# Optimization experiments

Hardware: AMD Instinct MI355X
Metric: run time of the kernel (lower is better)

The kernel has to match this reference:

```python
import jax, jax.numpy as jnp
import numpy as np

B, L, E = 2, 2048, 2048
H, KVH, HD = 16, 4, 128          # n_heads, n_kv_heads, head_dim = E // H
WIN = 512                        # window_size
SCALE = 1.0 / (HD ** 0.5)
NEG = -1e30


def setup_inputs() -> dict:
    key = jax.random.key(0)
    ks = jax.random.split(key, 5)
    s = 0.02
    return {
        "x":  jax.random.normal(ks[0], (B, L, E), dtype=jnp.float32),
        "Wq": jax.random.normal(ks[1], (E, H * HD), dtype=jnp.float32) * s,
        "Wk": jax.random.normal(ks[2], (E, KVH * HD), dtype=jnp.float32) * s,
        "Wv": jax.random.normal(ks[3], (E, KVH * HD), dtype=jnp.float32) * s,
        "Wo": jax.random.normal(ks[4], (H * HD, E), dtype=jnp.float32) * s,
    }


def reference(x, Wq, Wk, Wv, Wo):
    # projections
    q = (x @ Wq).reshape(B, L, H, HD)      # [B, L, H, HD]
    k = (x @ Wk).reshape(B, L, KVH, HD)    # [B, L, KVH, HD]
    v = (x @ Wv).reshape(B, L, KVH, HD)
    # GQA: expand kv heads (repeat_interleave over head dim)
    rep = H // KVH
    k = jnp.repeat(k, rep, axis=2)         # [B, L, H, HD]
    v = jnp.repeat(v, rep, axis=2)
    # scores [B, H, L, L]
    scores = jnp.einsum("bqhd,bkhd->bhqk", q, k) * SCALE
    i = jnp.arange(L)[:, None]
    j = jnp.arange(L)[None, :]
    mask = (j > i) | (j < i - WIN)         # True = masked
    scores = jnp.where(mask[None, None], NEG, scores)
    attn = jax.nn.softmax(scores, axis=-1)
    out = jnp.einsum("bhqk,bkhd->bqhd", attn, v).reshape(B, L, H * HD)
    return out @ Wo                        # [B, L, E]
```

## Files before the change

kernel.cpp:

```cpp
#include <hip/hip_runtime.h>
#include <hip/hip_bf16.h>
#include <type_traits>

#define B_ 2
#define L_ 2048
#define E_ 2048
#define H_ 16
#define KVH_ 4
#define HD_ 128
#define WIN_ 512
#define REP_ (H_ / KVH_)
#define SCALE_ 0.08838834764831843f

typedef __bf16 bf16x8 __attribute__((ext_vector_type(8)));
typedef float f32x4 __attribute__((ext_vector_type(4)));
typedef unsigned short u16x8 __attribute__((ext_vector_type(8)));

__device__ __forceinline__ unsigned short f2bf(float x) {
    __hip_bfloat16 h = __float2bfloat16(x);
    return *reinterpret_cast<unsigned short*>(&h);
}

__device__ __forceinline__ void gload_lds16(const unsigned short* g, unsigned short* l) {
    __builtin_amdgcn_global_load_lds(
        (const __attribute__((address_space(1))) void*)g,
        (__attribute__((address_space(3))) void*)l,
        16, 0, 0);
}

__global__ __launch_bounds__(256) void conv_f32_bf16(
        const float* __restrict__ in, unsigned short* __restrict__ out, int n4) {
    int i = blockIdx.x * 256 + threadIdx.x;
    if (i >= n4) return;
    float4 v = reinterpret_cast<const float4*>(in)[i];
    ushort4 o;
    o.x = f2bf(v.x); o.y = f2bf(v.y); o.z = f2bf(v.z); o.w = f2bf(v.w);
    reinterpret_cast<ushort4*>(out)[i] = o;
}

__global__ __launch_bounds__(256) void transpose_f32_bf16(
        const float* __restrict__ W, unsigned short* __restrict__ WT,
        int K, int N, int wts) {
    __shared__ unsigned short tile[32][33];
    const int t = threadIdx.x;
    const int r = t >> 5, c = t & 31;
    const int k0 = blockIdx.y * 32, n0 = blockIdx.x * 32;
    #pragma unroll
    for (int i = 0; i < 4; ++i)
        tile[r + i * 8][c] = f2bf(W[(size_t)(k0 + r + i * 8) * N + n0 + c]);
    __syncthreads();
    #pragma unroll
    for (int i = 0; i < 4; ++i)
        WT[(size_t)(n0 + r + i * 8) * wts + k0 + c] = tile[c][r + i * 8];
}

__global__ __launch_bounds__(256) void transpose_v_bf16(
        const unsigned short* __restrict__ kv, unsigned short* __restrict__ vT) {
    __shared__ unsigned short tile[32][33];
    const int t = threadIdx.x;
    const int r = t >> 5, c = t & 31;
    const int l0 = blockIdx.y * 32;
    const int n0 = blockIdx.x * 32;
    #pragma unroll
    for (int i = 0; i < 4; ++i)
        tile[r + i * 8][c] = kv[(size_t)(l0 + r + i * 8) * 1024 + 512 + n0 + c];
    __syncthreads();
    const int bq = l0 >> 11, lqv = l0 & 2047;
    #pragma unroll
    for (int i = 0; i < 4; ++i)
        vT[(size_t)(bq * 512 + n0 + r + i * 8) * (size_t)L_ + lqv + c] = tile[c][r + i * 8];
}

template<typename OT>
__global__ __launch_bounds__(256) void gemm_bt(
        const unsigned short* __restrict__ A, const unsigned short* __restrict__ BT,
        OT* __restrict__ C, int M, int N, int K) {
    __shared__ __attribute__((aligned(16))) unsigned short As[128 * 32];
    __shared__ __attribute__((aligned(16))) unsigned short Bs[128 * 32];
    const int t  = threadIdx.x;
    const int wv = t >> 6, ln = t & 63;
    const int wr = wv >> 1, wc = wv & 1;
    const int nwg = gridDim.x * gridDim.y;
    int lin = blockIdx.y * gridDim.x + blockIdx.x;
    if ((nwg & 7) == 0) lin = (lin & 7) * (nwg >> 3) + (lin >> 3);
    const int bm = (lin / gridDim.x) * 128, bn = (lin % gridDim.x) * 128;
    const int lrow = ln & 15;
    const int lk8  = (ln >> 4) * 8;

    f32x4 acc[4][4];
    const f32x4 z = {0.f, 0.f, 0.f, 0.f};
    #pragma unroll
    for (int m = 0; m < 4; ++m)
        #pragma unroll
        for (int n = 0; n < 4; ++n) acc[m][n] = z;

    for (int k0 = 0; k0 < K; k0 += 32) {
        #pragma unroll
        for (int seg = 0; seg < 2; ++seg) {
            const int chunk = seg * 256 + t;
            const int row = chunk >> 2, c8 = (chunk & 3) * 8;
            const int lbase = (seg * 256 + wv * 64) * 8;
            gload_lds16(A  + (size_t)(bm + row) * K + k0 + c8, &As[lbase]);
            gload_lds16(BT + (size_t)(bn + row) * K + k0 + c8, &Bs[lbase]);
        }
        __syncthreads();
        bf16x8 af[4], bfr[4];
        #pragma unroll
        for (int m = 0; m < 4; ++m)
            af[m] = *reinterpret_cast<const bf16x8*>(
                &As[(wr * 64 + m * 16 + lrow) * 32 + lk8]);
        #pragma unroll
        for (int n = 0; n < 4; ++n)
            bfr[n] = *reinterpret_cast<const bf16x8*>(
                &Bs[(wc * 64 + n * 16 + lrow) * 32 + lk8]);
        __builtin_amdgcn_s_setprio(1);
        #pragma unroll
        for (int m = 0; m < 4; ++m)
            #pragma unroll
            for (int n = 0; n < 4; ++n)
                acc[m][n] = __builtin_amdgcn_mfma_f32_16x16x32_bf16(
                    af[m], bfr[n], acc[m][n], 0, 0, 0);
        __builtin_amdgcn_s_setprio(0);
        __syncthreads();
    }
    const int crq = (ln >> 4) * 4;
    #pragma unroll
    for (int m = 0; m < 4; ++m)
        #pragma unroll
        for (int n = 0; n < 4; ++n)
            #pragma unroll
            for (int r = 0; r < 4; ++r) {
                size_t idx = (size_t)(bm + wr * 64 + m * 16 + crq + r) * N
                             + bn + wc * 64 + n * 16 + lrow;
                if constexpr (std::is_same_v<OT, float>) C[idx] = acc[m][n][r];
                else C[idx] = f2bf(acc[m][n][r]);
            }
}

__global__ __launch_bounds__(256) void attn_mfma(
        const unsigned short* __restrict__ qb,
        const unsigned short* __restrict__ kvb,
        const unsigned short* __restrict__ vT,
        unsigned short* __restrict__ ob) {
    __shared__ __attribute__((aligned(16))) unsigned short Ks[32 * 128];
    __shared__ __attribute__((aligned(16))) unsigned short VsT[128 * 40];

    const int t  = threadIdx.x;
    const int w  = t >> 6, l = t & 63;
    const int lin = blockIdx.y * gridDim.x + blockIdx.x;
    const int wid = (lin & 7) * 128 + (lin >> 3);
    const int bh  = wid >> 5;
    const int qt  = 31 - (wid & 31);
    const int b  = bh >> 4, h = bh & 15;
    const int kh = h >> 2;
    const int i0 = qt * 64;
    const int iw = i0 + w * 16;
    const int lq = l & 15;
    const int g  = l >> 4;
    const int g8 = g * 8;
    const int i  = iw + lq;

    bf16x8 qf[4];
    {
        const unsigned short* qrow = qb + (size_t)(b * L_ + iw + lq) * E_ + h * HD_;
        #pragma unroll
        for (int dc = 0; dc < 4; ++dc)
            qf[dc] = *reinterpret_cast<const bf16x8*>(qrow + dc * 32 + g8);
    }

    f32x4 oacc[8];
    const f32x4 z = {0.f, 0.f, 0.f, 0.f};
    #pragma unroll
    for (int c = 0; c < 8; ++c) oacc[c] = z;
    float mreg = -50000.f, lreg = 0.f;

    int jlo = i0 - WIN_; if (jlo < 0) jlo = 0;
    const int nch = (i0 + 64 - jlo) >> 5;
    const int wlo = iw - WIN_, whi = iw + 15;
    const unsigned short* vbase = vT + (size_t)((b * KVH_ + kh) * HD_) * L_;

    for (int ch = 0; ch < nch; ++ch) {
        const int jb = jlo + ch * 32;
        #pragma unroll
        for (int s = 0; s < 2; ++s) {
            const int e  = t + s * 256;
            const int kr = e >> 4;
            const int d8 = (e & 15) * 8;
            u16x8 kk = *reinterpret_cast<const u16x8*>(
                kvb + (size_t)(b * L_ + jb + kr) * 1024 + kh * HD_ + d8);
            *reinterpret_cast<u16x8*>(&Ks[kr * 128 + (d8 ^ ((kr & 7) << 3))]) = kk;
            const int dv = e >> 2;
            const int k8 = (e & 3) * 8;
            u16x8 vv = *reinterpret_cast<const u16x8*>(
                vbase + (size_t)dv * L_ + jb + k8);
            *reinterpret_cast<u16x8*>(&VsT[dv * 40 + k8]) = vv;
        }
        __syncthreads();

        if (jb + 31 >= wlo && jb <= whi) {
            f32x4 st[2]; st[0] = z; st[1] = z;
            __builtin_amdgcn_s_setprio(1);
            #pragma unroll
            for (int kt = 0; kt < 2; ++kt) {
                const int krow = kt * 16 + lq;
                #pragma unroll
                for (int dc = 0; dc < 4; ++dc) {
                    bf16x8 kf = *reinterpret_cast<const bf16x8*>(
                        &Ks[krow * 128 + ((dc * 32 + g8) ^ ((krow & 7) << 3))]);
                    st[kt] = __builtin_amdgcn_mfma_f32_16x16x32_bf16(
                        kf, qf[dc], st[kt], 0, 0, 0);
                }
            }
            __builtin_amdgcn_s_setprio(0);
            float p8[2][4];
            float cmax = -1e30f;
            #pragma unroll
            for (int kt = 0; kt < 2; ++kt)
                #pragma unroll
                for (int r = 0; r < 4; ++r) {
                    const int j = jb + kt * 16 + g * 4 + r;
                    float s = st[kt][r] * SCALE_;
                    s = (j <= i && j >= i - WIN_) ? s : -1e30f;
                    p8[kt][r] = s;
                    cmax = fmaxf(cmax, s);
                }
            cmax = fmaxf(cmax, __shfl_xor(cmax, 16));
            cmax = fmaxf(cmax, __shfl_xor(cmax, 32));
            const bool noresc = __all(cmax - mreg <= 8.f);
            float alpha = 1.f;
            if (!noresc) {
                const float mnew = fmaxf(mreg, cmax);
                alpha = __expf(mreg - mnew);
                mreg = mnew;
            }
            float psum = 0.f;
            #pragma unroll
            for (int kt = 0; kt < 2; ++kt)
                #pragma unroll
                for (int r = 0; r < 4; ++r) {
                    const float p = __expf(p8[kt][r] - mreg);
                    p8[kt][r] = p; psum += p;
                }
            psum += __shfl_xor(psum, 16);
            psum += __shfl_xor(psum, 32);
            if (noresc) {
                lreg += psum;
            } else {
                lreg = lreg * alpha + psum;
                #pragma unroll
                for (int c = 0; c < 8; ++c)
                    #pragma unroll
                    for (int r = 0; r < 4; ++r) oacc[c][r] *= alpha;
            }
            const unsigned u00 = ((unsigned)f2bf(p8[0][1]) << 16) | f2bf(p8[0][0]);
            const unsigned u01 = ((unsigned)f2bf(p8[0][3]) << 16) | f2bf(p8[0][2]);
            const unsigned u10 = ((unsigned)f2bf(p8[1][1]) << 16) | f2bf(p8[1][0]);
            const unsigned u11 = ((unsigned)f2bf(p8[1][3]) << 16) | f2bf(p8[1][2]);
            union { unsigned u[4]; bf16x8 v; } pu;
            #pragma unroll
            for (int wd = 0; wd < 4; ++wd) {
                const int src = ((g & 1) * 2 + (wd >> 1)) * 16 + lq;
                const unsigned a0 = __shfl(wd & 1 ? u01 : u00, src);
                const unsigned a1 = __shfl(wd & 1 ? u11 : u10, src);
                pu.u[wd] = (g < 2) ? a0 : a1;
            }
            const bf16x8 pb = pu.v;
            __builtin_amdgcn_s_setprio(1);
            #pragma unroll
            for (int c = 0; c < 8; ++c) {
                bf16x8 af = *reinterpret_cast<const bf16x8*>(
                    &VsT[(c * 16 + lq) * 40 + g8]);
                oacc[c] = __builtin_amdgcn_mfma_f32_16x16x32_bf16(
                    af, pb, oacc[c], 0, 0, 0);
            }
            __builtin_amdgcn_s_setprio(0);
        }
        __syncthreads();
    }

    const float inv = 1.f / lreg;
    unsigned short* orow = ob + (size_t)(b * L_ + iw + lq) * E_ + h * HD_;
    #pragma unroll
    for (int c = 0; c < 8; ++c) {
        ushort4 o4;
        o4.x = f2bf(oacc[c][0] * inv);
        o4.y = f2bf(oacc[c][1] * inv);
        o4.z = f2bf(oacc[c][2] * inv);
        o4.w = f2bf(oacc[c][3] * inv);
        *reinterpret_cast<ushort4*>(&orow[c * 16 + g * 4]) = o4;
    }
}

extern "C" void kernel_launch(void* const* d_in, const int* in_sizes, int n_in,
                              void* d_out, int out_size, void* d_ws, size_t ws_size,
                              hipStream_t stream) {
    const float* x  = (const float*)d_in[0];
    const float* Wq = (const float*)d_in[1];
    const float* Wk = (const float*)d_in[2];
    const float* Wv = (const float*)d_in[3];
    const float* Wo = (const float*)d_in[4];
    float* out = (float*)d_out;

    const int M = B_ * L_;
    char* w = (char*)d_ws;
    unsigned short* qbuf  = (unsigned short*)w; w += (size_t)M * E_ * 2;
    unsigned short* kvbuf = (unsigned short*)w; w += (size_t)M * 1024 * 2;
    unsigned short* xb    = (unsigned short*)w; w += (size_t)M * E_ * 2;
    unsigned short* wT1   = (unsigned short*)w; w += (size_t)E_ * E_ * 2;
    unsigned short* wkvT  = (unsigned short*)w; w += (size_t)1024 * E_ * 2;
    unsigned short* vTb   = (unsigned short*)w; w += (size_t)1024 * L_ * 2;

    dim3 blk(256);

    conv_f32_bf16<<<dim3((M * E_ / 4 + 255) / 256), blk, 0, stream>>>(x, xb, M * E_ / 4);
    transpose_f32_bf16<<<dim3(E_ / 32, E_ / 32), blk, 0, stream>>>(Wq, wT1, E_, E_, E_);
    transpose_f32_bf16<<<dim3(512 / 32, E_ / 32), blk, 0, stream>>>(Wk, wkvT, E_, 512, E_);
    transpose_f32_bf16<<<dim3(512 / 32, E_ / 32), blk, 0, stream>>>(Wv, wkvT + (size_t)512 * E_, E_, 512, E_);

    gemm_bt<unsigned short><<<dim3(E_ / 128, M / 128), blk, 0, stream>>>(
        xb, wT1, qbuf, M, E_, E_);
    gemm_bt<unsigned short><<<dim3(1024 / 128, M / 128), blk, 0, stream>>>(
        xb, wkvT, kvbuf, M, 1024, E_);

    transpose_v_bf16<<<dim3(512 / 32, M / 32), blk, 0, stream>>>(kvbuf, vTb);

    attn_mfma<<<dim3(L_ / 64, B_ * H_), blk, 0, stream>>>(qbuf, kvbuf, vTb, xb);

    transpose_f32_bf16<<<dim3(E_ / 32, E_ / 32), blk, 0, stream>>>(Wo, wT1, E_, E_, E_);
    gemm_bt<float><<<dim3(E_ / 128, M / 128), blk, 0, stream>>>(xb, wT1, out, M, E_, E_);
}
```

Before: 344.5 us.

## Fuse QKV projections into one GEMM and double-buffer K/V tiles in attention

```diff
diff --git a/kernel.cpp b/kernel.cpp
--- a/kernel.cpp
+++ b/kernel.cpp
@@ -11,6 +11,7 @@
 #define WIN_ 512
 #define REP_ (H_ / KVH_)
 #define SCALE_ 0.08838834764831843f
+#define QKVP_ 3072
 
 typedef __bf16 bf16x8 __attribute__((ext_vector_type(8)));
 typedef float f32x4 __attribute__((ext_vector_type(4)));
@@ -54,8 +55,28 @@
         WT[(size_t)(n0 + r + i * 8) * wts + k0 + c] = tile[c][r + i * 8];
 }
 
+__global__ __launch_bounds__(256) void transpose_wqkv(
+        const float* __restrict__ Wq, const float* __restrict__ Wk,
+        const float* __restrict__ Wv, unsigned short* __restrict__ WT) {
+    __shared__ unsigned short tile[32][33];
+    const int t = threadIdx.x;
+    const int r = t >> 5, c = t & 31;
+    const int n0 = blockIdx.x * 32, k0 = blockIdx.y * 32;
+    const float* src; int scol, sN;
+    if (n0 < 2048)      { src = Wq; scol = n0;        sN = 2048; }
+    else if (n0 < 2560) { src = Wk; scol = n0 - 2048; sN = 512;  }
+    else                { src = Wv; scol = n0 - 2560; sN = 512;  }
+    #pragma unroll
+    for (int i = 0; i < 4; ++i)
+        tile[r + i * 8][c] = f2bf(src[(size_t)(k0 + r + i * 8) * sN + scol + c]);
+    __syncthreads();
+    #pragma unroll
+    for (int i = 0; i < 4; ++i)
+        WT[(size_t)(n0 + r + i * 8) * 2048 + k0 + c] = tile[c][r + i * 8];
+}
+
 __global__ __launch_bounds__(256) void transpose_v_bf16(
-        const unsigned short* __restrict__ kv, unsigned short* __restrict__ vT) {
+        const unsigned short* __restrict__ qkv, unsigned short* __restrict__ vT) {
     __shared__ unsigned short tile[32][33];
     const int t = threadIdx.x;
     const int r = t >> 5, c = t & 31;
@@ -63,7 +84,7 @@
     const int n0 = blockIdx.x * 32;
     #pragma unroll
     for (int i = 0; i < 4; ++i)
-        tile[r + i * 8][c] = kv[(size_t)(l0 + r + i * 8) * 1024 + 512 + n0 + c];
+        tile[r + i * 8][c] = qkv[(size_t)(l0 + r + i * 8) * QKVP_ + 2560 + n0 + c];
     __syncthreads();
     const int bq = l0 >> 11, lqv = l0 & 2047;
     #pragma unroll
@@ -138,12 +159,11 @@
 }
 
 __global__ __launch_bounds__(256) void attn_mfma(
-        const unsigned short* __restrict__ qb,
-        const unsigned short* __restrict__ kvb,
+        const unsigned short* __restrict__ qkv,
         const unsigned short* __restrict__ vT,
         unsigned short* __restrict__ ob) {
-    __shared__ __attribute__((aligned(16))) unsigned short Ks[32 * 128];
-    __shared__ __attribute__((aligned(16))) unsigned short VsT[128 * 40];
+    __shared__ __attribute__((aligned(16))) unsigned short Ks[2][32 * 128];
+    __shared__ __attribute__((aligned(16))) unsigned short VsT[2][128 * 40];
 
     const int t  = threadIdx.x;
     const int w  = t >> 6, l = t & 63;
@@ -160,9 +180,16 @@
     const int g8 = g * 8;
     const int i  = iw + lq;
 
+    const int kr  = t >> 4;
+    const int d8  = (t & 15) * 8;
+    const int dv0 = t >> 2;
+    const int k8  = (t & 3) * 8;
+    const unsigned short* kbase = qkv + (size_t)(b * L_) * QKVP_ + 2048 + kh * HD_;
+    const unsigned short* vbase = vT + (size_t)((b * KVH_ + kh) * HD_) * L_;
+
     bf16x8 qf[4];
     {
-        const unsigned short* qrow = qb + (size_t)(b * L_ + iw + lq) * E_ + h * HD_;
+        const unsigned short* qrow = qkv + (size_t)(b * L_ + iw + lq) * QKVP_ + h * HD_;
         #pragma unroll
         for (int dc = 0; dc < 4; ++dc)
             qf[dc] = *reinterpret_cast<const bf16x8*>(qrow + dc * 32 + g8);
@@ -177,25 +204,32 @@
     int jlo = i0 - WIN_; if (jlo < 0) jlo = 0;
     const int nch = (i0 + 64 - jlo) >> 5;
     const int wlo = iw - WIN_, whi = iw + 15;
-    const unsigned short* vbase = vT + (size_t)((b * KVH_ + kh) * HD_) * L_;
-
+
+    {
+        const int jb = jlo;
+        u16x8 k0 = *(const u16x8*)(kbase + (size_t)(jb + kr) * QKVP_ + d8);
+        u16x8 k1 = *(const u16x8*)(kbase + (size_t)(jb + kr + 16) * QKVP_ + d8);
+        u16x8 v0 = *(const u16x8*)(vbase + (size_t)dv0 * L_ + jb + k8);
+        u16x8 v1 = *(const u16x8*)(vbase + (size_t)(dv0 + 64) * L_ + jb + k8);
+        *(u16x8*)&Ks[0][kr * 128 + (d8 ^ ((kr & 7) << 3))] = k0;
+        *(u16x8*)&Ks[0][(kr + 16) * 128 + (d8 ^ ((kr & 7) << 3))] = k1;
+        *(u16x8*)&VsT[0][dv0 * 40 + k8] = v0;
+        *(u16x8*)&VsT[0][(dv0 + 64) * 40 + k8] = v1;
+    }
+    __syncthreads();
+
+    int cur = 0;
     for (int ch = 0; ch < nch; ++ch) {
         const int jb = jlo + ch * 32;
-        #pragma unroll
-        for (int s = 0; s < 2; ++s) {
-            const int e  = t + s * 256;
-            const int kr = e >> 4;
-            const int d8 = (e & 15) * 8;
-            u16x8 kk = *reinterpret_cast<const u16x8*>(
-                kvb + (size_t)(b * L_ + jb + kr) * 1024 + kh * HD_ + d8);
-            *reinterpret_cast<u16x8*>(&Ks[kr * 128 + (d8 ^ ((kr & 7) << 3))]) = kk;
-            const int dv = e >> 2;
-            const int k8 = (e & 3) * 8;
-            u16x8 vv = *reinterpret_cast<const u16x8*>(
-                vbase + (size_t)dv * L_ + jb + k8);
-            *reinterpret_cast<u16x8*>(&VsT[dv * 40 + k8]) = vv;
+        const bool pre = (ch + 1 < nch);
+        u16x8 k0, k1, v0, v1;
+        if (pre) {
+            const int jn = jb + 32;
+            k0 = *(const u16x8*)(kbase + (size_t)(jn + kr) * QKVP_ + d8);
+            k1 = *(const u16x8*)(kbase + (size_t)(jn + kr + 16) * QKVP_ + d8);
+            v0 = *(const u16x8*)(vbase + (size_t)dv0 * L_ + jn + k8);
+            v1 = *(const u16x8*)(vbase + (size_t)(dv0 + 64) * L_ + jn + k8);
         }
-        __syncthreads();
 
         if (jb + 31 >= wlo && jb <= whi) {
             f32x4 st[2]; st[0] = z; st[1] = z;
@@ -206,7 +240,7 @@
                 #pragma unroll
                 for (int dc = 0; dc < 4; ++dc) {
                     bf16x8 kf = *reinterpret_cast<const bf16x8*>(
-                        &Ks[krow * 128 + ((dc * 32 + g8) ^ ((krow & 7) << 3))]);
+                        &Ks[cur][krow * 128 + ((dc * 32 + g8) ^ ((krow & 7) << 3))]);
                     st[kt] = __builtin_amdgcn_mfma_f32_16x16x32_bf16(
                         kf, qf[dc], st[kt], 0, 0, 0);
                 }
@@ -269,13 +303,22 @@
             #pragma unroll
             for (int c = 0; c < 8; ++c) {
                 bf16x8 af = *reinterpret_cast<const bf16x8*>(
-                    &VsT[(c * 16 + lq) * 40 + g8]);
+                    &VsT[cur][(c * 16 + lq) * 40 + g8]);
                 oacc[c] = __builtin_amdgcn_mfma_f32_16x16x32_bf16(
                     af, pb, oacc[c], 0, 0, 0);
             }
             __builtin_amdgcn_s_setprio(0);
         }
+
+        if (pre) {
+            const int nb = cur ^ 1;
+            *(u16x8*)&Ks[nb][kr * 128 + (d8 ^ ((kr & 7) << 3))] = k0;
+            *(u16x8*)&Ks[nb][(kr + 16) * 128 + (d8 ^ ((kr & 7) << 3))] = k1;
+            *(u16x8*)&VsT[nb][dv0 * 40 + k8] = v0;
+            *(u16x8*)&VsT[nb][(dv0 + 64) * 40 + k8] = v1;
+        }
         __syncthreads();
+        cur ^= 1;
     }
 
     const float inv = 1.f / lreg;
@@ -303,29 +346,24 @@
 
     const int M = B_ * L_;
     char* w = (char*)d_ws;
-    unsigned short* qbuf  = (unsigned short*)w; w += (size_t)M * E_ * 2;
-    unsigned short* kvbuf = (unsigned short*)w; w += (size_t)M * 1024 * 2;
+    unsigned short* qkv   = (unsigned short*)w; w += (size_t)M * QKVP_ * 2;
     unsigned short* xb    = (unsigned short*)w; w += (size_t)M * E_ * 2;
+    unsigned short* wqkvT = (unsigned short*)w; w += (size_t)QKVP_ * E_ * 2;
     unsigned short* wT1   = (unsigned short*)w; w += (size_t)E_ * E_ * 2;
-    unsigned short* wkvT  = (unsigned short*)w; w += (size_t)1024 * E_ * 2;
     unsigned short* vTb   = (unsigned short*)w; w += (size_t)1024 * L_ * 2;
 
     dim3 blk(256);
 
     conv_f32_bf16<<<dim3((M * E_ / 4 + 255) / 256), blk, 0, stream>>>(x, xb, M * E_ / 4);
-    transpose_f32_bf16<<<dim3(E_ / 32, E_ / 32), blk, 0, stream>>>(Wq, wT1, E_, E_, E_);
-    transpose_f32_bf16<<<dim3(512 / 32, E_ / 32), blk, 0, stream>>>(Wk, wkvT, E_, 512, E_);
-    transpose_f32_bf16<<<dim3(512 / 32, E_ / 32), blk, 0, stream>>>(Wv, wkvT + (size_t)512 * E_, E_, 512, E_);
-
-    gemm_bt<unsigned short><<<dim3(E_ / 128, M / 128), blk, 0, stream>>>(
-        xb, wT1, qbuf, M, E_, E_);
-    gemm_bt<unsigned short><<<dim3(1024 / 128, M / 128), blk, 0, stream>>>(
-        xb, wkvT, kvbuf, M, 1024, E_);
-
-    transpose_v_bf16<<<dim3(512 / 32, M / 32), blk, 0, stream>>>(kvbuf, vTb);
-
-    attn_mfma<<<dim3(L_ / 64, B_ * H_), blk, 0, stream>>>(qbuf, kvbuf, vTb, xb);
-
+    transpose_wqkv<<<dim3(QKVP_ / 32, E_ / 32), blk, 0, stream>>>(Wq, Wk, Wv, wqkvT);
     transpose_f32_bf16<<<dim3(E_ / 32, E_ / 32), blk, 0, stream>>>(Wo, wT1, E_, E_, E_);
+
+    gemm_bt<unsigned short><<<dim3(QKVP_ / 128, M / 128), blk, 0, stream>>>(
+        xb, wqkvT, qkv, M, QKVP_, E_);
+
+    transpose_v_bf16<<<dim3(512 / 32, M / 32), blk, 0, stream>>>(qkv, vTb);
+
+    attn_mfma<<<dim3(L_ / 64, B_ * H_), blk, 0, stream>>>(qkv, vTb, xb);
+
     gemm_bt<float><<<dim3(E_ / 128, M / 128), blk, 0, stream>>>(xb, wT1, out, M, E_, E_);
 }
```

Result: faster. 303.4 us (-12.0%).
